# Optimization experiments

Measured on AMD Instinct MI355X. Metric: run time of the kernel, lower is better.

## Reference

```python
import jax, jax.numpy as jnp
import numpy as np

E, H, I, TOPK = 16, 2048, 1408, 4
B, S = 2, 1024


def setup_inputs() -> dict:
    key = jax.random.key(0)
    ks = jax.random.split(key, 6)
    hidden_states = jax.random.normal(ks[0], (B, S, H), dtype=jnp.float32)
    topk_idx = jax.random.randint(ks[1], (B, S, TOPK), 0, E)
    topk_weight = jax.random.uniform(ks[2], (B, S, TOPK), dtype=jnp.float32) / TOPK
    gate_weight = jax.random.normal(ks[3], (E, I, H), dtype=jnp.float32) * (1.0 / np.sqrt(H))
    up_weight = jax.random.normal(ks[4], (E, I, H), dtype=jnp.float32) * (1.0 / np.sqrt(H))
    down_weight = jax.random.normal(ks[5], (E, H, I), dtype=jnp.float32) * (1.0 / np.sqrt(I))
    return {
        "hidden_states": hidden_states,
        "topk_idx": topk_idx,
        "topk_weight": topk_weight,
        "gate_weight": gate_weight,
        "up_weight": up_weight,
        "down_weight": down_weight,
    }


def reference(hidden_states, topk_idx, topk_weight, gate_weight, up_weight, down_weight):
    b, s, h = hidden_states.shape
    n_tokens = b * s
    topk = topk_idx.shape[-1]
    x = hidden_states.reshape(n_tokens, h)

    flat_expert = topk_idx.reshape(-1)                      # (P,) P = n_tokens*topk
    flat_weight = topk_weight.reshape(-1).astype(hidden_states.dtype)

    # Sort dispatched (token, expert) pairs by expert id -> contiguous expert groups.
    perm = jnp.argsort(flat_expert)                          # stable sort
    tok = jnp.repeat(jnp.arange(n_tokens), topk)[perm]       # source token per sorted row
    xs = x[tok]                                              # (P, H) gathered expert inputs
    group_sizes = jnp.bincount(flat_expert, length=E).astype(jnp.int32)

    # Grouped GEMMs: rhs laid out (E, in, out); nn.Linear weight is (out, in).
    gate = jax.lax.ragged_dot(xs, jnp.swapaxes(gate_weight, 1, 2), group_sizes)  # (P, I)
    up = jax.lax.ragged_dot(xs, jnp.swapaxes(up_weight, 1, 2), group_sizes)      # (P, I)
    h_act = jax.nn.silu(gate) * up
    down = jax.lax.ragged_dot(h_act, jnp.swapaxes(down_weight, 1, 2), group_sizes)  # (P, H)

    # Weighted scatter-combine back to tokens.
    w_sorted = flat_weight[perm]
    out = jnp.zeros((n_tokens, h), hidden_states.dtype).at[tok].add(down * w_sorted[:, None])
    return out.reshape(b, s, h)
```

## Files before the change

kernel.cpp:

```cpp
#include <hip/hip_runtime.h>


#define NE   16
#define HD   2048
#define ID   1408
#define NTOK 2048
#define NP   8192
#define MAXT 96

typedef _Float16 f16x8 __attribute__((ext_vector_type(8)));
typedef float    f32x4 __attribute__((ext_vector_type(4)));
typedef unsigned short u16;
typedef u16      u16x8 __attribute__((ext_vector_type(8)));

__device__ __forceinline__ u16 f2hu(float f) {
  _Float16 h = (_Float16)f;
  return __builtin_bit_cast(u16, h);
}

__device__ __forceinline__ void gl2lds16(const void* g, void* l) {
  __builtin_amdgcn_global_load_lds((__attribute__((address_space(1))) void*)(void*)(g),
                                   (__attribute__((address_space(3))) void*)(l),
                                   16, 0, 0);
}

__global__ void k_route(const int* __restrict__ idx, const float* __restrict__ w,
                        int* __restrict__ slot_tok, float* __restrict__ slot_w,
                        int* __restrict__ tinfo) {
  __shared__ int hist[NE], cur[NE];
  int t = threadIdx.x;
  if (t < NE) hist[t] = 0;
  __syncthreads();
  for (int p = t; p < NP; p += 256) atomicAdd(&hist[idx[p]], 1);
  __syncthreads();
  if (t == 0) {
    int acc = 0, nt = 0;
    for (int e = 0; e < NE; ++e) {
      int c = hist[e];
      cur[e] = acc;
      for (int m = 0; m < c; m += 128) {
        tinfo[1 + nt*3 + 0] = e;
        tinfo[1 + nt*3 + 1] = acc + m;
        tinfo[1 + nt*3 + 2] = (c - m < 128) ? (c - m) : 128;
        ++nt;
      }
      acc += c;
    }
    tinfo[0] = nt;
  }
  __syncthreads();
  for (int p = t; p < NP; p += 256) {
    int e = idx[p];
    int s = atomicAdd(&cur[e], 1);
    slot_tok[s] = p >> 2;
    slot_w[s]   = w[p];
  }
}

__global__ void k_gather(const float* __restrict__ x, const int* __restrict__ slot_tok,
                         u16* __restrict__ xs) {
  int s = blockIdx.x;
  int tok = slot_tok[s];
  const float* src = x + (size_t)tok * HD;
  u16* dst = xs + (size_t)s * HD;
  int c = threadIdx.x * 8;
  float4 a = *(const float4*)(src + c);
  float4 b = *(const float4*)(src + c + 4);
  u16x8 o;
  o[0]=f2hu(a.x); o[1]=f2hu(a.y); o[2]=f2hu(a.z); o[3]=f2hu(a.w);
  o[4]=f2hu(b.x); o[5]=f2hu(b.y); o[6]=f2hu(b.z); o[7]=f2hu(b.w);
  *(u16x8*)(dst + c) = o;
}

__global__ void k_cvt(const float* __restrict__ s, u16* __restrict__ d, int n) {
  long i = ((long)blockIdx.x * blockDim.x + threadIdx.x) * 8;
  long stride = (long)gridDim.x * blockDim.x * 8;
  for (; i < n; i += stride) {
    float4 a = *(const float4*)(s + i);
    float4 b = *(const float4*)(s + i + 4);
    u16x8 o;
    o[0]=f2hu(a.x); o[1]=f2hu(a.y); o[2]=f2hu(a.z); o[3]=f2hu(a.w);
    o[4]=f2hu(b.x); o[5]=f2hu(b.y); o[6]=f2hu(b.z); o[7]=f2hu(b.w);
    *(u16x8*)(d + i) = o;
  }
}

__global__ __launch_bounds__(256, 2)
void k_gateup(const u16* __restrict__ xs, const u16* __restrict__ wg,
              const u16* __restrict__ wu, u16* __restrict__ hact,
              const int* __restrict__ tinfo) {
  int flat = blockIdx.x;
  int swz  = (flat & 7) * 110 + (flat >> 3);
  int mt   = swz % 80;
  int nt   = swz / 80;
  if (mt >= tinfo[0]) return;
  int e  = tinfo[1 + mt*3 + 0];
  int m0 = tinfo[1 + mt*3 + 1];
  int mc = tinfo[1 + mt*3 + 2];
  int n0 = nt * 128;

  const u16* wgb = wg + (size_t)e * ID * HD;
  const u16* wub = wu + (size_t)e * ID * HD;

  __shared__ __align__(16) char As[128*64*2];
  __shared__ __align__(16) char Gs[128*64*2];
  __shared__ __align__(16) char Us[128*64*2];

  int t = threadIdx.x;
  int lane = t & 63, wave = t >> 6;
  int wm = (wave >> 1) * 64, wn = (wave & 1) * 64;
  int rlo = lane & 15, quad = lane >> 4;

  const u16* pA[4]; const u16* pG[4]; const u16* pU[4];
#pragma unroll
  for (int r = 0; r < 4; ++r) {
    int row = r*32 + (t >> 3);
    int cg  = (t & 7) ^ (row & 7);
    int ar  = row < mc ? row : mc - 1;
    pA[r] = xs  + (size_t)(m0 + ar)  * HD + cg*8;
    pG[r] = wgb + (size_t)(n0 + row) * HD + cg*8;
    pU[r] = wub + (size_t)(n0 + row) * HD + cg*8;
  }
  int ldsu = wave * 1024;

  f32x4 accg[4][4], accu[4][4];
  const f32x4 fz = {0.f, 0.f, 0.f, 0.f};
#pragma unroll
  for (int i = 0; i < 4; ++i)
#pragma unroll
    for (int j = 0; j < 4; ++j) { accg[i][j] = fz; accu[i][j] = fz; }

  for (int kt = 0; kt < HD; kt += 64) {
#pragma unroll
    for (int r = 0; r < 4; ++r) {
      gl2lds16(pA[r] + kt, As + r*4096 + ldsu);
      gl2lds16(pG[r] + kt, Gs + r*4096 + ldsu);
      gl2lds16(pU[r] + kt, Us + r*4096 + ldsu);
    }
    __builtin_amdgcn_s_waitcnt(0);
    __syncthreads();

#pragma unroll
    for (int ks = 0; ks < 2; ++ks) {
      f16x8 av[4], gv[4], uv[4];
#pragma unroll
      for (int f = 0; f < 4; ++f) {
        int rA = wm + f*16 + rlo;
        int rB = wn + f*16 + rlo;
        int cA = (((ks*4 + quad) ^ (rA & 7))) * 16;
        int cB = (((ks*4 + quad) ^ (rB & 7))) * 16;
        av[f] = *(const f16x8*)(As + rA*128 + cA);
        gv[f] = *(const f16x8*)(Gs + rB*128 + cB);
        uv[f] = *(const f16x8*)(Us + rB*128 + cB);
      }
#pragma unroll
      for (int fm = 0; fm < 4; ++fm)
#pragma unroll
        for (int fn = 0; fn < 4; ++fn) {
          accg[fm][fn] = __builtin_amdgcn_mfma_f32_16x16x32_f16(av[fm], gv[fn], accg[fm][fn], 0, 0, 0);
          accu[fm][fn] = __builtin_amdgcn_mfma_f32_16x16x32_f16(av[fm], uv[fn], accu[fm][fn], 0, 0, 0);
        }
    }
    __syncthreads();
  }

#pragma unroll
  for (int fm = 0; fm < 4; ++fm) {
    int mb = wm + fm*16 + quad*4;
#pragma unroll
    for (int rr = 0; rr < 4; ++rr) {
      int m = mb + rr;
      if (m < mc) {
        u16* drow = hact + (size_t)(m0 + m) * ID + n0 + wn + rlo;
#pragma unroll
        for (int fn = 0; fn < 4; ++fn) {
          float g = accg[fm][fn][rr];
          float u = accu[fm][fn][rr];
          float hv = (g / (1.f + __expf(-g))) * u;
          drow[fn*16] = f2hu(hv);
        }
      }
    }
  }
}

__global__ __launch_bounds__(256, 3)
void k_down(const u16* __restrict__ ha, const u16* __restrict__ wd,
            float* __restrict__ out, const int* __restrict__ slot_tok,
            const float* __restrict__ slot_w, const int* __restrict__ tinfo) {
  int flat = blockIdx.x;
  int swz  = (flat & 7) * 160 + (flat >> 3);
  int mt   = swz % 80;
  int nt   = swz / 80;
  if (mt >= tinfo[0]) return;
  int e  = tinfo[1 + mt*3 + 0];
  int m0 = tinfo[1 + mt*3 + 1];
  int mc = tinfo[1 + mt*3 + 2];
  int n0 = nt * 128;

  const u16* wb = wd + (size_t)e * HD * ID;

  __shared__ __align__(16) char As[128*64*2];
  __shared__ __align__(16) char Bs[128*64*2];

  int t = threadIdx.x;
  int lane = t & 63, wave = t >> 6;
  int wm = (wave >> 1) * 64, wn = (wave & 1) * 64;
  int rlo = lane & 15, quad = lane >> 4;

  const u16* pA[4]; const u16* pB[4];
#pragma unroll
  for (int r = 0; r < 4; ++r) {
    int row = r*32 + (t >> 3);
    int cg  = (t & 7) ^ (row & 7);
    int ar  = row < mc ? row : mc - 1;
    pA[r] = ha + (size_t)(m0 + ar)  * ID + cg*8;
    pB[r] = wb + (size_t)(n0 + row) * ID + cg*8;
  }
  int ldsu = wave * 1024;

  f32x4 acc[4][4];
  const f32x4 fz = {0.f, 0.f, 0.f, 0.f};
#pragma unroll
  for (int i = 0; i < 4; ++i)
#pragma unroll
    for (int j = 0; j < 4; ++j) acc[i][j] = fz;

  for (int kt = 0; kt < ID; kt += 64) {
#pragma unroll
    for (int r = 0; r < 4; ++r) {
      gl2lds16(pA[r] + kt, As + r*4096 + ldsu);
      gl2lds16(pB[r] + kt, Bs + r*4096 + ldsu);
    }
    __builtin_amdgcn_s_waitcnt(0);
    __syncthreads();

#pragma unroll
    for (int ks = 0; ks < 2; ++ks) {
      f16x8 av[4], bv[4];
#pragma unroll
      for (int f = 0; f < 4; ++f) {
        int rA = wm + f*16 + rlo;
        int rB = wn + f*16 + rlo;
        int cA = (((ks*4 + quad) ^ (rA & 7))) * 16;
        int cB = (((ks*4 + quad) ^ (rB & 7))) * 16;
        av[f] = *(const f16x8*)(As + rA*128 + cA);
        bv[f] = *(const f16x8*)(Bs + rB*128 + cB);
      }
#pragma unroll
      for (int fm = 0; fm < 4; ++fm)
#pragma unroll
        for (int fn = 0; fn < 4; ++fn)
          acc[fm][fn] = __builtin_amdgcn_mfma_f32_16x16x32_f16(av[fm], bv[fn], acc[fm][fn], 0, 0, 0);
    }
    __syncthreads();
  }

#pragma unroll
  for (int fm = 0; fm < 4; ++fm) {
    int mb = wm + fm*16 + quad*4;
#pragma unroll
    for (int rr = 0; rr < 4; ++rr) {
      int m = mb + rr;
      if (m < mc) {
        int s = m0 + m;
        int tok = slot_tok[s];
        float w = slot_w[s];
        float* orow = out + (size_t)tok * HD + n0 + wn + rlo;
#pragma unroll
        for (int fn = 0; fn < 4; ++fn)
          atomicAdd(orow + fn*16, acc[fm][fn][rr] * w);
      }
    }
  }
}

extern "C" void kernel_launch(void* const* d_in, const int* in_sizes, int n_in,
                              void* d_out, int out_size, void* d_ws, size_t ws_size,
                              hipStream_t stream) {
  (void)in_sizes; (void)n_in; (void)out_size; (void)ws_size;
  const float* hs   = (const float*)d_in[0];
  const int*   tidx = (const int*)d_in[1];
  const float* tw   = (const float*)d_in[2];
  const float* gw   = (const float*)d_in[3];
  const float* uw   = (const float*)d_in[4];
  const float* dw   = (const float*)d_in[5];
  float* out = (float*)d_out;

  char* ws = (char*)d_ws;
  size_t off = 0;
  auto carve = [&](size_t b) { char* p = ws + off; off += (b + 255) & ~(size_t)255; return p; };
  u16* xs    = (u16*)carve((size_t)NP * HD * 2);
  u16* wgh   = (u16*)carve((size_t)NE * ID * HD * 2);
  u16* wuh   = (u16*)carve((size_t)NE * ID * HD * 2);
  u16* wdh   = (u16*)carve((size_t)NE * HD * ID * 2);
  u16* hact  = (u16*)carve((size_t)NP * ID * 2);
  int*   slot_tok = (int*)carve((size_t)NP * 4);
  float* slot_w   = (float*)carve((size_t)NP * 4);
  int*   tinfo    = (int*)carve((size_t)(1 + MAXT*3) * 4);

  hipMemsetAsync(out, 0, (size_t)NTOK * HD * 4, stream);
  k_route<<<1, 256, 0, stream>>>(tidx, tw, slot_tok, slot_w, tinfo);
  int wn_el = NE * ID * HD;
  k_cvt<<<4096, 256, 0, stream>>>(dw, wdh, wn_el);
  k_cvt<<<4096, 256, 0, stream>>>(gw, wgh, wn_el);
  k_cvt<<<4096, 256, 0, stream>>>(uw, wuh, wn_el);
  k_gather<<<NP, 256, 0, stream>>>(hs, slot_tok, xs);
  k_gateup<<<dim3(880), 256, 0, stream>>>(xs, wgh, wuh, hact, tinfo);
  k_down  <<<dim3(1280), 256, 0, stream>>>(hact, wdh, out, slot_tok, slot_w, tinfo);
}
```

Measured before the change: 827.1 us.

## Fuse fp32-to-fp16 weight conversion into grouped GEMM tile loads

Removes the three standalone weight conversion kernels and their fp16 workspace copies. The gate/up and down GEMMs now load fp32 weights straight from global memory into registers, convert them to fp16 and store them into LDS in the existing swizzled layout. This avoids a full read-convert-write pass over all expert weights, at the cost of twice the weight bytes per tile load, loss of the async global-to-LDS path for the weights, and higher register pressure (k_down occupancy hint lowered to 2).

```diff
diff --git a/kernel.cpp b/kernel.cpp
--- a/kernel.cpp
+++ b/kernel.cpp
@@ -16,6 +16,13 @@
 __device__ __forceinline__ u16 f2hu(float f) {
   _Float16 h = (_Float16)f;
   return __builtin_bit_cast(u16, h);
+}
+
+__device__ __forceinline__ f16x8 cvt8(float4 a, float4 b) {
+  f16x8 o;
+  o[0]=(_Float16)a.x; o[1]=(_Float16)a.y; o[2]=(_Float16)a.z; o[3]=(_Float16)a.w;
+  o[4]=(_Float16)b.x; o[5]=(_Float16)b.y; o[6]=(_Float16)b.z; o[7]=(_Float16)b.w;
+  return o;
 }
 
 __device__ __forceinline__ void gl2lds16(const void* g, void* l) {
@@ -72,22 +79,9 @@
   *(u16x8*)(dst + c) = o;
 }
 
-__global__ void k_cvt(const float* __restrict__ s, u16* __restrict__ d, int n) {
-  long i = ((long)blockIdx.x * blockDim.x + threadIdx.x) * 8;
-  long stride = (long)gridDim.x * blockDim.x * 8;
-  for (; i < n; i += stride) {
-    float4 a = *(const float4*)(s + i);
-    float4 b = *(const float4*)(s + i + 4);
-    u16x8 o;
-    o[0]=f2hu(a.x); o[1]=f2hu(a.y); o[2]=f2hu(a.z); o[3]=f2hu(a.w);
-    o[4]=f2hu(b.x); o[5]=f2hu(b.y); o[6]=f2hu(b.z); o[7]=f2hu(b.w);
-    *(u16x8*)(d + i) = o;
-  }
-}
-
 __global__ __launch_bounds__(256, 2)
-void k_gateup(const u16* __restrict__ xs, const u16* __restrict__ wg,
-              const u16* __restrict__ wu, u16* __restrict__ hact,
+void k_gateup(const u16* __restrict__ xs, const float* __restrict__ wg,
+              const float* __restrict__ wu, u16* __restrict__ hact,
               const int* __restrict__ tinfo) {
   int flat = blockIdx.x;
   int swz  = (flat & 7) * 110 + (flat >> 3);
@@ -99,8 +93,8 @@
   int mc = tinfo[1 + mt*3 + 2];
   int n0 = nt * 128;
 
-  const u16* wgb = wg + (size_t)e * ID * HD;
-  const u16* wub = wu + (size_t)e * ID * HD;
+  const float* wgb = wg + (size_t)e * ID * HD;
+  const float* wub = wu + (size_t)e * ID * HD;
 
   __shared__ __align__(16) char As[128*64*2];
   __shared__ __align__(16) char Gs[128*64*2];
@@ -111,7 +105,7 @@
   int wm = (wave >> 1) * 64, wn = (wave & 1) * 64;
   int rlo = lane & 15, quad = lane >> 4;
 
-  const u16* pA[4]; const u16* pG[4]; const u16* pU[4];
+  const u16* pA[4]; const float* pG[4]; const float* pU[4];
 #pragma unroll
   for (int r = 0; r < 4; ++r) {
     int row = r*32 + (t >> 3);
@@ -132,10 +126,23 @@
 
   for (int kt = 0; kt < HD; kt += 64) {
 #pragma unroll
+    for (int r = 0; r < 4; ++r)
+      gl2lds16(pA[r] + kt, As + r*4096 + ldsu);
+
+    f16x8 gst[4], ust[4];
+#pragma unroll
     for (int r = 0; r < 4; ++r) {
-      gl2lds16(pA[r] + kt, As + r*4096 + ldsu);
-      gl2lds16(pG[r] + kt, Gs + r*4096 + ldsu);
-      gl2lds16(pU[r] + kt, Us + r*4096 + ldsu);
+      float4 g0 = *(const float4*)(pG[r] + kt);
+      float4 g1 = *(const float4*)(pG[r] + kt + 4);
+      float4 u0 = *(const float4*)(pU[r] + kt);
+      float4 u1 = *(const float4*)(pU[r] + kt + 4);
+      gst[r] = cvt8(g0, g1);
+      ust[r] = cvt8(u0, u1);
+    }
+#pragma unroll
+    for (int r = 0; r < 4; ++r) {
+      *(f16x8*)(Gs + r*4096 + t*16) = gst[r];
+      *(f16x8*)(Us + r*4096 + t*16) = ust[r];
     }
     __builtin_amdgcn_s_waitcnt(0);
     __syncthreads();
@@ -184,8 +191,8 @@
   }
 }
 
-__global__ __launch_bounds__(256, 3)
-void k_down(const u16* __restrict__ ha, const u16* __restrict__ wd,
+__global__ __launch_bounds__(256, 2)
+void k_down(const u16* __restrict__ ha, const float* __restrict__ wd,
             float* __restrict__ out, const int* __restrict__ slot_tok,
             const float* __restrict__ slot_w, const int* __restrict__ tinfo) {
   int flat = blockIdx.x;
@@ -198,7 +205,7 @@
   int mc = tinfo[1 + mt*3 + 2];
   int n0 = nt * 128;
 
-  const u16* wb = wd + (size_t)e * HD * ID;
+  const float* wb = wd + (size_t)e * HD * ID;
 
   __shared__ __align__(16) char As[128*64*2];
   __shared__ __align__(16) char Bs[128*64*2];
@@ -208,7 +215,7 @@
   int wm = (wave >> 1) * 64, wn = (wave & 1) * 64;
   int rlo = lane & 15, quad = lane >> 4;
 
-  const u16* pA[4]; const u16* pB[4];
+  const u16* pA[4]; const float* pB[4];
 #pragma unroll
   for (int r = 0; r < 4; ++r) {
     int row = r*32 + (t >> 3);
@@ -228,10 +235,20 @@
 
   for (int kt = 0; kt < ID; kt += 64) {
 #pragma unroll
+    for (int r = 0; r < 4; ++r)
+      gl2lds16(pA[r] + kt, As + r*4096 + ldsu);
+
+    f16x8 bst[4];
+#pragma unroll
     for (int r = 0; r < 4; ++r) {
-      gl2lds16(pA[r] + kt, As + r*4096 + ldsu);
-      gl2lds16(pB[r] + kt, Bs + r*4096 + ldsu);
-    }
+      float4 b0 = *(const float4*)(pB[r] + kt);
+      float4 b1 = *(const float4*)(pB[r] + kt + 4);
+      bst[r] = cvt8(b0, b1);
+    }
+#pragma unroll
+    for (int r = 0; r < 4; ++r)
+      *(f16x8*)(Bs + r*4096 + t*16) = bst[r];
+
     __builtin_amdgcn_s_waitcnt(0);
     __syncthreads();
 
@@ -291,9 +308,6 @@
   size_t off = 0;
   auto carve = [&](size_t b) { char* p = ws + off; off += (b + 255) & ~(size_t)255; return p; };
   u16* xs    = (u16*)carve((size_t)NP * HD * 2);
-  u16* wgh   = (u16*)carve((size_t)NE * ID * HD * 2);
-  u16* wuh   = (u16*)carve((size_t)NE * ID * HD * 2);
-  u16* wdh   = (u16*)carve((size_t)NE * HD * ID * 2);
   u16* hact  = (u16*)carve((size_t)NP * ID * 2);
   int*   slot_tok = (int*)carve((size_t)NP * 4);
   float* slot_w   = (float*)carve((size_t)NP * 4);
@@ -301,11 +315,7 @@
 
   hipMemsetAsync(out, 0, (size_t)NTOK * HD * 4, stream);
   k_route<<<1, 256, 0, stream>>>(tidx, tw, slot_tok, slot_w, tinfo);
-  int wn_el = NE * ID * HD;
-  k_cvt<<<4096, 256, 0, stream>>>(dw, wdh, wn_el);
-  k_cvt<<<4096, 256, 0, stream>>>(gw, wgh, wn_el);
-  k_cvt<<<4096, 256, 0, stream>>>(uw, wuh, wn_el);
   k_gather<<<NP, 256, 0, stream>>>(hs, slot_tok, xs);
-  k_gateup<<<dim3(880), 256, 0, stream>>>(xs, wgh, wuh, hact, tinfo);
-  k_down  <<<dim3(1280), 256, 0, stream>>>(hact, wdh, out, slot_tok, slot_w, tinfo);
-}
+  k_gateup<<<dim3(880), 256, 0, stream>>>(xs, gw, uw, hact, tinfo);
+  k_down  <<<dim3(1280), 256, 0, stream>>>(hact, dw, out, slot_tok, slot_w, tinfo);
+}
```

Measured after the change: 815.5 us. Within noise of the previous version (-1.4%).
